# Kernel optimization log

Measured on AMD Instinct MI355X. Metric: run time of the kernel, lower is better.

## Reference

```python
import jax, jax.numpy as jnp
import numpy as np


def _bilinear_sample(fea, px, py):
    # fea: [C,H,W]; px,py: [D,H,W] pixel coords (align_corners=True, zeros padding)
    C, H, W = fea.shape
    x0 = jnp.floor(px); y0 = jnp.floor(py)
    wx = px - x0; wy = py - y0
    x0i = x0.astype(jnp.int32); y0i = y0.astype(jnp.int32)

    def g(xi, yi):
        valid = (xi >= 0) & (xi < W) & (yi >= 0) & (yi < H)
        v = fea[:, jnp.clip(yi, 0, H - 1), jnp.clip(xi, 0, W - 1)]  # [C,D,H,W]
        return jnp.where(valid[None], v, 0.0)

    return (g(x0i, y0i) * ((1 - wx) * (1 - wy))[None]
            + g(x0i + 1, y0i) * (wx * (1 - wy))[None]
            + g(x0i, y0i + 1) * ((1 - wx) * wy)[None]
            + g(x0i + 1, y0i + 1) * (wx * wy)[None])


def homo_warping_3d(src_fea, src_proj, ref_proj, depth_values):
    # src_fea [B,C,H,W]; src_proj/ref_proj [B,4,4]; depth_values [B,D] -> [B,C,D,H,W]
    B, C, H, W = src_fea.shape
    D = depth_values.shape[1]
    proj = src_proj @ jnp.linalg.inv(ref_proj)
    rot, trans = proj[:, :3, :3], proj[:, :3, 3]
    yy, xx = jnp.meshgrid(jnp.arange(H, dtype=src_fea.dtype),
                          jnp.arange(W, dtype=src_fea.dtype), indexing='ij')
    xyz = jnp.stack([xx.ravel(), yy.ravel(), jnp.ones(H * W, src_fea.dtype)], 0)  # [3,HW]
    rot_xyz = jnp.einsum('bij,jp->bip', rot, xyz)  # [B,3,HW]
    pxyz = rot_xyz[:, :, None, :] * depth_values[:, None, :, None] + trans[:, :, None, None]
    xy = pxyz[:, :2] / pxyz[:, 2:3]
    # grid is computed under torch.no_grad() in the original
    px = jax.lax.stop_gradient(xy[:, 0].reshape(B, D, H, W))
    py = jax.lax.stop_gradient(xy[:, 1].reshape(B, D, H, W))
    return jax.vmap(_bilinear_sample)(src_fea, px, py)  # [B,C,D,H,W]


def conf_regression(p, n=4):
    # sliding sum of n consecutive depth probabilities, gathered at expected depth index
    B, D, H, W = p.shape
    pad = jnp.pad(p, ((0, 0), (1, 2), (0, 0), (0, 0)))  # [B,D+3,H,W]
    cs = jnp.cumsum(pad, axis=1)
    cs = jnp.concatenate([jnp.zeros_like(cs[:, :1]), cs], axis=1)  # [B,D+4,H,W]
    sum_n = cs[:, n:n + D] - cs[:, 0:D]  # [B,D,H,W]
    d_idx = jnp.sum(p * jnp.arange(D, dtype=p.dtype)[None, :, None, None], axis=1)
    idx = jnp.clip(d_idx.astype(jnp.int32), 0, D - 1)
    return jnp.take_along_axis(sum_n, idx[:, None], axis=1)[:, 0]


def reference(ref_feats, src_feats, proj_matrices, depth_values, num_depth, w_reg):
    V = proj_matrices.shape[1]
    assert ref_feats.shape[0] == V - 1 and depth_values.shape[1] == num_depth
    ref_proj = proj_matrices[:, 0]
    ref_proj_new = ref_proj[:, 0].at[:, :3, :4].set(ref_proj[:, 1, :3, :3] @ ref_proj[:, 0, :3, :4])
    volume_sum = 0.0
    for v in range(V - 1):
        src_proj = proj_matrices[:, v + 1]
        src_proj_new = src_proj[:, 0].at[:, :3, :4].set(src_proj[:, 1, :3, :3] @ src_proj[:, 0, :3, :4])
        warped = homo_warping_3d(src_feats[v], src_proj_new, ref_proj_new, depth_values)
        volume_sum = volume_sum + ref_feats[v][:, :, None] * warped  # [B,C,D,H,W]
    volume_mean = volume_sum / (V - 1)
    # cost regularization: bias-free 3x3x3 3D conv C->1
    cost = jax.lax.conv_general_dilated(volume_mean, w_reg, (1, 1, 1), 'SAME',
                                        dimension_numbers=('NCDHW', 'OIDHW', 'NCDHW'))
    prob_volume = jax.nn.softmax(cost[:, 0], axis=1)  # [B,D,H,W]
    depth = jnp.sum(prob_volume * depth_values[:, :, None, None], axis=1)  # [B,H,W]
    conf = jax.lax.stop_gradient(conf_regression(prob_volume))  # [B,H,W]
    return depth, conf


def setup_inputs() -> dict:
    key = jax.random.key(0)
    B, V, C, D, H, W = 1, 5, 32, 48, 128, 160
    k1, k2, k3 = jax.random.split(key, 3)
    ref_feats = jax.random.normal(k1, (V - 1, B, C, H, W), jnp.float32)
    src_feats = jax.random.normal(k2, (V - 1, B, C, H, W), jnp.float32)
    # geometrically valid cameras: index 0 = extrinsic 4x4, index 1 = intrinsic 4x4
    f = 200.0
    K = np.eye(4, dtype=np.float32)
    K[0, 0] = f; K[1, 1] = f; K[0, 2] = W / 2.0; K[1, 2] = H / 2.0
    projs = np.zeros((B, V, 2, 4, 4), np.float32)
    for v in range(V):
        ang = 0.04 * v
        R = np.array([[np.cos(ang), 0, np.sin(ang)], [0, 1, 0], [-np.sin(ang), 0, np.cos(ang)]], np.float32)
        E = np.eye(4, dtype=np.float32)
        E[:3, :3] = R
        E[:3, 3] = np.array([-40.0 * v, 0.0, 0.0], np.float32)
        projs[:, v, 0] = E
        projs[:, v, 1] = K
    depth_values = jnp.broadcast_to(jnp.linspace(425.0, 935.0, D, dtype=jnp.float32)[None], (B, D))
    w_reg = jax.random.normal(k3, (1, C, 3, 3, 3), jnp.float32) * 0.05
    return {"ref_feats": ref_feats, "src_feats": src_feats,
            "proj_matrices": jnp.asarray(projs), "depth_values": depth_values,
            "num_depth": D, "w_reg": w_reg}
```

## Files before the change

kernel.cpp:

```cpp
#include <hip/hip_runtime.h>
#include <math.h>

#define H_ 128
#define W_ 160
#define D_ 48
#define C_ 32
#define K27 27
#define HW_ (H_ * W_)
#define DHW_ (D_ * HW_)
#define CHW_ (C_ * HW_)

typedef float f4 __attribute__((ext_vector_type(4)));

__device__ __forceinline__ void build_proj(const float* __restrict__ P, int v,
                                           double M[4][4]) {
    const float* E = P + (v * 2 + 0) * 16;
    const float* K = P + (v * 2 + 1) * 16;
    for (int i = 0; i < 3; i++)
        for (int j = 0; j < 4; j++) {
            double s = 0.0;
            for (int k = 0; k < 3; k++) s += (double)K[i * 4 + k] * (double)E[k * 4 + j];
            M[i][j] = s;
        }
    for (int j = 0; j < 4; j++) M[3][j] = (double)E[12 + j];
}

__global__ void proj_kernel(const float* __restrict__ P, float* __restrict__ rt) {
    if (threadIdx.x != 0) return;
    double M0[4][4];
    build_proj(P, 0, M0);
    double a[4][8];
    for (int i = 0; i < 4; i++)
        for (int j = 0; j < 4; j++) {
            a[i][j] = M0[i][j];
            a[i][4 + j] = (i == j) ? 1.0 : 0.0;
        }
    for (int col = 0; col < 4; ++col) {
        int piv = col;
        double best = fabs(a[col][col]);
        for (int r = col + 1; r < 4; r++) {
            double vv = fabs(a[r][col]);
            if (vv > best) { best = vv; piv = r; }
        }
        if (piv != col)
            for (int j = 0; j < 8; j++) {
                double t = a[col][j]; a[col][j] = a[piv][j]; a[piv][j] = t;
            }
        double inv = 1.0 / a[col][col];
        for (int j = 0; j < 8; j++) a[col][j] *= inv;
        for (int r = 0; r < 4; r++)
            if (r != col) {
                double f = a[r][col];
                for (int j = 0; j < 8; j++) a[r][j] -= f * a[col][j];
            }
    }
    double Minv[4][4];
    for (int i = 0; i < 4; i++)
        for (int j = 0; j < 4; j++) Minv[i][j] = a[i][4 + j];

    for (int v = 1; v < 5; ++v) {
        double Mv[4][4];
        build_proj(P, v, Mv);
        double Pm[4][4];
        for (int i = 0; i < 4; i++)
            for (int j = 0; j < 4; j++) {
                double s = 0.0;
                for (int k = 0; k < 4; k++) s += Mv[i][k] * Minv[k][j];
                Pm[i][j] = s;
            }
        float* o = rt + (v - 1) * 12;
        o[0] = (float)Pm[0][0]; o[1] = (float)Pm[0][1]; o[2] = (float)Pm[0][2];
        o[3] = (float)Pm[1][0]; o[4] = (float)Pm[1][1]; o[5] = (float)Pm[1][2];
        o[6] = (float)Pm[2][0]; o[7] = (float)Pm[2][1]; o[8] = (float)Pm[2][2];
        o[9] = (float)Pm[0][3]; o[10] = (float)Pm[1][3]; o[11] = (float)Pm[2][3];
    }
}

__global__ void transpose_kernel(const float* __restrict__ in,
                                 float* __restrict__ out) {
    int t = blockIdx.x * blockDim.x + threadIdx.x;
    if (t >= 4 * HW_) return;
    int pix = t % HW_;
    int v = t / HW_;
    float vals[C_];
#pragma unroll
    for (int c = 0; c < C_; c++) vals[c] = in[(size_t)v * CHW_ + c * HW_ + pix];
    f4* o = (f4*)(out + ((size_t)v * HW_ + pix) * C_);
#pragma unroll
    for (int q = 0; q < 8; q++) {
        f4 w = {vals[4 * q], vals[4 * q + 1], vals[4 * q + 2], vals[4 * q + 3]};
        o[q] = w;
    }
}

__global__ void __launch_bounds__(256)
warp_fold_x_kernel(const float* __restrict__ srcT,
                   const float* __restrict__ refT,
                   const float* __restrict__ rt,
                   const float* __restrict__ dvals,
                   const float* __restrict__ wreg,
                   float* __restrict__ Gx) {
    __shared__ float accT[8][64][4];
    __shared__ float gLDS[K27][164];

    int t = threadIdx.x;
    int blk = blockIdx.x;
    int d = blk >> 7;
    int y = blk & 127;
    float depth = dvals[d];
    float yf = (float)y;
    int rowbase = d * HW_ + y * W_;

#pragma unroll 1
    for (int b = 0; b < 3; b++) {
        int vox = t >> 2;
        int cgrp = t & 3;
        int vg = b * 64 + vox;
        int x = vg - 1;

        f4 acc0 = (f4){0.f, 0.f, 0.f, 0.f};
        f4 acc1 = (f4){0.f, 0.f, 0.f, 0.f};

        if (x >= 0 && x < W_) {
            float xf = (float)x;
            int pix = y * W_ + x;
#pragma unroll 2
            for (int v = 0; v < 4; v++) {
                const float* m = rt + v * 12;
                float px = fmaf(fmaf(m[0], xf, fmaf(m[1], yf, m[2])), depth, m[9]);
                float py = fmaf(fmaf(m[3], xf, fmaf(m[4], yf, m[5])), depth, m[10]);
                float pz = fmaf(fmaf(m[6], xf, fmaf(m[7], yf, m[8])), depth, m[11]);
                float iz = 1.f / pz;
                px *= iz;
                py *= iz;
                float x0f = floorf(px), y0f = floorf(py);
                float wx = px - x0f, wy = py - y0f;
                int x0 = (int)x0f, y0 = (int)y0f;
                int x1 = x0 + 1, y1 = y0 + 1;

                float w00 = (1.f - wx) * (1.f - wy);
                float w10 = wx * (1.f - wy);
                float w01 = (1.f - wx) * wy;
                float w11 = wx * wy;
                bool vx0 = (x0 >= 0) && (x0 < W_);
                bool vx1 = (x1 >= 0) && (x1 < W_);
                bool vy0 = (y0 >= 0) && (y0 < H_);
                bool vy1 = (y1 >= 0) && (y1 < H_);
                if (!(vx0 && vy0)) w00 = 0.f;
                if (!(vx1 && vy0)) w10 = 0.f;
                if (!(vx0 && vy1)) w01 = 0.f;
                if (!(vx1 && vy1)) w11 = 0.f;
                int cx0 = min(max(x0, 0), W_ - 1);
                int cx1 = min(max(x1, 0), W_ - 1);
                int cy0 = min(max(y0, 0), H_ - 1);
                int cy1 = min(max(y1, 0), H_ - 1);

                const f4* p00 = (const f4*)(srcT + ((size_t)v * HW_ + cy0 * W_ + cx0) * C_ + cgrp * 8);
                const f4* p10 = (const f4*)(srcT + ((size_t)v * HW_ + cy0 * W_ + cx1) * C_ + cgrp * 8);
                const f4* p01 = (const f4*)(srcT + ((size_t)v * HW_ + cy1 * W_ + cx0) * C_ + cgrp * 8);
                const f4* p11 = (const f4*)(srcT + ((size_t)v * HW_ + cy1 * W_ + cx1) * C_ + cgrp * 8);
                const f4* pr  = (const f4*)(refT + ((size_t)v * HW_ + pix) * C_ + cgrp * 8);

                f4 a00 = p00[0], b00 = p00[1];
                f4 a10 = p10[0], b10 = p10[1];
                f4 a01 = p01[0], b01 = p01[1];
                f4 a11 = p11[0], b11 = p11[1];
                f4 r0 = pr[0],  r1 = pr[1];

                f4 sv0 = a00 * w00 + a10 * w10 + a01 * w01 + a11 * w11;
                f4 sv1 = b00 * w00 + b10 * w10 + b01 * w01 + b11 * w11;
                acc0 += r0 * sv0;
                acc1 += r1 * sv1;
            }
            acc0 *= 0.25f;
            acc1 *= 0.25f;
        }

        int cq0 = cgrp * 2;
        *(f4*)&accT[cq0][vox][0] = acc0;
        *(f4*)&accT[cq0 + 1][vox][0] = acc1;
        __syncthreads();

        int fvox = t & 63;
        int kg = t >> 6;
        int fvg = b * 64 + fvox;
        float av[C_];
#pragma unroll
        for (int cq = 0; cq < 8; cq++)
            *(f4*)&av[cq * 4] = *(const f4*)&accT[cq][fvox][0];

        if (fvg < 162) {
            int kstart = kg * 7;
            int kend = min(kstart + 7, K27);
#pragma unroll 1
            for (int k = kstart; k < kend; k++) {
                int ku = __builtin_amdgcn_readfirstlane(k);
                float g = 0.f;
#pragma unroll
                for (int c = 0; c < C_; c++) g = fmaf(wreg[c * K27 + ku], av[c], g);
                gLDS[ku][fvg] = g;
            }
        }
        __syncthreads();
    }

    if (t < W_) {
        int x = t;
#pragma unroll
        for (int j = 0; j < 9; j++) {
            float s = gLDS[j * 3 + 0][x] + gLDS[j * 3 + 1][x + 1] +
                      gLDS[j * 3 + 2][x + 2];
            Gx[(size_t)j * DHW_ + rowbase + x] = s;
        }
    }
}

__global__ void gather9_kernel(const float* __restrict__ Gx,
                               float* __restrict__ cost) {
    int t = blockIdx.x * blockDim.x + threadIdx.x;
    if (t >= DHW_ / 4) return;
    int idx = t * 4;
    int x = idx % W_;
    int y = (idx / W_) % H_;
    int d = idx / HW_;
    f4 acc = (f4){0.f, 0.f, 0.f, 0.f};
#pragma unroll
    for (int kd = 0; kd < 3; kd++) {
        int dd = d + kd - 1;
        if ((unsigned)dd >= (unsigned)D_) continue;
#pragma unroll
        for (int kh = 0; kh < 3; kh++) {
            int yy = y + kh - 1;
            if ((unsigned)yy >= (unsigned)H_) continue;
            int j = kd * 3 + kh;
            acc += *(const f4*)(Gx + (size_t)j * DHW_ + dd * HW_ + yy * W_ + x);
        }
    }
    *(f4*)(cost + idx) = acc;
}

__global__ void softmax_kernel(const float* __restrict__ cost,
                               const float* __restrict__ dvals,
                               float* __restrict__ out) {
    int pix = blockIdx.x * blockDim.x + threadIdx.x;
    if (pix >= HW_) return;
    float mx = -1e30f;
#pragma unroll 1
    for (int d = 0; d < D_; d++) mx = fmaxf(mx, cost[d * HW_ + pix]);
    float s = 0.f, dnum = 0.f, inum = 0.f;
#pragma unroll 1
    for (int d = 0; d < D_; d++) {
        float e = __expf(cost[d * HW_ + pix] - mx);
        s += e;
        dnum = fmaf(e, dvals[d], dnum);
        inum = fmaf(e, (float)d, inum);
    }
    float invs = 1.f / s;
    float depth = dnum * invs;
    float didx = inum * invs;
    int id = (int)didx;
    id = min(max(id, 0), D_ - 1);
    float conf = 0.f;
    for (int k = id - 1; k <= id + 2; ++k)
        if (k >= 0 && k < D_) conf += __expf(cost[k * HW_ + pix] - mx);
    conf *= invs;
    out[pix] = depth;
    out[HW_ + pix] = conf;
}

extern "C" void kernel_launch(void* const* d_in, const int* in_sizes, int n_in,
                              void* d_out, int out_size, void* d_ws, size_t ws_size,
                              hipStream_t stream) {
    const float* ref_feats = (const float*)d_in[0];
    const float* src_feats = (const float*)d_in[1];
    const float* proj      = (const float*)d_in[2];
    const float* dvals     = (const float*)d_in[3];
    const float* wreg      = (const float*)d_in[5];
    float* out = (float*)d_out;

    char* ws = (char*)d_ws;
    float* rt   = (float*)ws;
    float* srcT = (float*)(ws + 1024);
    float* refT = srcT + (size_t)4 * HW_ * C_;
    float* Gx   = refT + (size_t)4 * HW_ * C_;
    float* cost = Gx + (size_t)9 * DHW_;

    proj_kernel<<<1, 64, 0, stream>>>(proj, rt);
    transpose_kernel<<<(4 * HW_) / 256, 256, 0, stream>>>(src_feats, srcT);
    transpose_kernel<<<(4 * HW_) / 256, 256, 0, stream>>>(ref_feats, refT);
    warp_fold_x_kernel<<<D_ * H_, 256, 0, stream>>>(srcT, refT, rt, dvals, wreg, Gx);
    gather9_kernel<<<(DHW_ / 4) / 256, 256, 0, stream>>>(Gx, cost);
    softmax_kernel<<<HW_ / 256, 256, 0, stream>>>(cost, dvals, out);
}
```

Measured before the change: 217.2 us.

## Share per-view warp coordinates via shuffles, merge transposes, vectorize softmax

In the warp kernel, each of the four lanes serving a voxel now computes the projection and bilinear weights and offsets for one view, using per-row constants hoisted out of the loop. The results are broadcast to the other lanes with wave shuffles, so the projection math is not repeated four times per voxel. The two feature transposes become one launch, and the softmax kernel handles four pixels per thread with vector loads. The cost is eight shuffles per view iteration and fewer threads in the softmax, which lowers its parallelism.

Result: faster. 212.4 us (-2.2%).

```diff
diff --git a/kernel.cpp b/kernel.cpp
--- a/kernel.cpp
+++ b/kernel.cpp
@@ -76,10 +76,18 @@
     }
 }
 
-__global__ void transpose_kernel(const float* __restrict__ in,
-                                 float* __restrict__ out) {
+__global__ void transpose2_kernel(const float* __restrict__ sf,
+                                  const float* __restrict__ rf,
+                                  float* __restrict__ so,
+                                  float* __restrict__ ro) {
     int t = blockIdx.x * blockDim.x + threadIdx.x;
-    if (t >= 4 * HW_) return;
+    const float* in = sf;
+    float* out = so;
+    if (t >= 4 * HW_) {
+        t -= 4 * HW_;
+        in = rf;
+        out = ro;
+    }
     int pix = t % HW_;
     int v = t / HW_;
     float vals[C_];
@@ -104,6 +112,10 @@
     __shared__ float gLDS[K27][164];
 
     int t = threadIdx.x;
+    int lane = t & 63;
+    int qb = lane & 60;
+    int vox = t >> 2;
+    int cgrp = t & 3;
     int blk = blockIdx.x;
     int d = blk >> 7;
     int y = blk & 127;
@@ -111,55 +123,77 @@
     float yf = (float)y;
     int rowbase = d * HW_ + y * W_;
 
+    const float* m = rt + cgrp * 12;
+    float Ax = fmaf(fmaf(m[1], yf, m[2]), depth, m[9]);
+    float Bx = m[0] * depth;
+    float Ay = fmaf(fmaf(m[4], yf, m[5]), depth, m[10]);
+    float By = m[3] * depth;
+    float Az = fmaf(fmaf(m[7], yf, m[8]), depth, m[11]);
+    float Bz = m[6] * depth;
+
 #pragma unroll 1
     for (int b = 0; b < 3; b++) {
-        int vox = t >> 2;
-        int cgrp = t & 3;
         int vg = b * 64 + vox;
         int x = vg - 1;
+        bool xvalid = (x >= 0) && (x < W_);
+
+        float W00, W10, W01, W11;
+        int O00, O10, O01, O11;
+        {
+            float xf = (float)x;
+            float pz = fmaf(Bz, xf, Az);
+            float iz = 1.f / pz;
+            float px = fmaf(Bx, xf, Ax) * iz;
+            float py = fmaf(By, xf, Ay) * iz;
+            float x0f = floorf(px), y0f = floorf(py);
+            float wx = px - x0f, wy = py - y0f;
+            int x0 = (int)x0f, y0 = (int)y0f;
+            int x1 = x0 + 1, y1 = y0 + 1;
+            W00 = (1.f - wx) * (1.f - wy);
+            W10 = wx * (1.f - wy);
+            W01 = (1.f - wx) * wy;
+            W11 = wx * wy;
+            bool vx0 = (x0 >= 0) && (x0 < W_);
+            bool vx1 = (x1 >= 0) && (x1 < W_);
+            bool vy0 = (y0 >= 0) && (y0 < H_);
+            bool vy1 = (y1 >= 0) && (y1 < H_);
+            if (!(vx0 && vy0)) W00 = 0.f;
+            if (!(vx1 && vy0)) W10 = 0.f;
+            if (!(vx0 && vy1)) W01 = 0.f;
+            if (!(vx1 && vy1)) W11 = 0.f;
+            int cx0 = min(max(x0, 0), W_ - 1);
+            int cx1 = min(max(x1, 0), W_ - 1);
+            int cy0 = min(max(y0, 0), H_ - 1);
+            int cy1 = min(max(y1, 0), H_ - 1);
+            O00 = (cy0 * W_ + cx0) * C_;
+            O10 = (cy0 * W_ + cx1) * C_;
+            O01 = (cy1 * W_ + cx0) * C_;
+            O11 = (cy1 * W_ + cx1) * C_;
+        }
 
         f4 acc0 = (f4){0.f, 0.f, 0.f, 0.f};
         f4 acc1 = (f4){0.f, 0.f, 0.f, 0.f};
 
-        if (x >= 0 && x < W_) {
-            float xf = (float)x;
+        if (xvalid) {
             int pix = y * W_ + x;
+            const float* rbase = refT + (size_t)pix * C_ + cgrp * 8;
 #pragma unroll 2
             for (int v = 0; v < 4; v++) {
-                const float* m = rt + v * 12;
-                float px = fmaf(fmaf(m[0], xf, fmaf(m[1], yf, m[2])), depth, m[9]);
-                float py = fmaf(fmaf(m[3], xf, fmaf(m[4], yf, m[5])), depth, m[10]);
-                float pz = fmaf(fmaf(m[6], xf, fmaf(m[7], yf, m[8])), depth, m[11]);
-                float iz = 1.f / pz;
-                px *= iz;
-                py *= iz;
-                float x0f = floorf(px), y0f = floorf(py);
-                float wx = px - x0f, wy = py - y0f;
-                int x0 = (int)x0f, y0 = (int)y0f;
-                int x1 = x0 + 1, y1 = y0 + 1;
-
-                float w00 = (1.f - wx) * (1.f - wy);
-                float w10 = wx * (1.f - wy);
-                float w01 = (1.f - wx) * wy;
-                float w11 = wx * wy;
-                bool vx0 = (x0 >= 0) && (x0 < W_);
-                bool vx1 = (x1 >= 0) && (x1 < W_);
-                bool vy0 = (y0 >= 0) && (y0 < H_);
-                bool vy1 = (y1 >= 0) && (y1 < H_);
-                if (!(vx0 && vy0)) w00 = 0.f;
-                if (!(vx1 && vy0)) w10 = 0.f;
-                if (!(vx0 && vy1)) w01 = 0.f;
-                if (!(vx1 && vy1)) w11 = 0.f;
-                int cx0 = min(max(x0, 0), W_ - 1);
-                int cx1 = min(max(x1, 0), W_ - 1);
-                int cy0 = min(max(y0, 0), H_ - 1);
-                int cy1 = min(max(y1, 0), H_ - 1);
-
-                const f4* p00 = (const f4*)(srcT + ((size_t)v * HW_ + cy0 * W_ + cx0) * C_ + cgrp * 8);
-                const f4* p10 = (const f4*)(srcT + ((size_t)v * HW_ + cy0 * W_ + cx1) * C_ + cgrp * 8);
-                const f4* p01 = (const f4*)(srcT + ((size_t)v * HW_ + cy1 * W_ + cx0) * C_ + cgrp * 8);
-                const f4* p11 = (const f4*)(srcT + ((size_t)v * HW_ + cy1 * W_ + cx1) * C_ + cgrp * 8);
-                const f4* pr  = (const f4*)(refT + ((size_t)v * HW_ + pix) * C_ + cgrp * 8);
+                float w00 = __shfl(W00, qb + v);
+                float w10 = __shfl(W10, qb + v);
+                float w01 = __shfl(W01, qb + v);
+                float w11 = __shfl(W11, qb + v);
+                int o00 = __shfl(O00, qb + v);
+                int o10 = __shfl(O10, qb + v);
+                int o01 = __shfl(O01, qb + v);
+                int o11 = __shfl(O11, qb + v);
+
+                const float* sv = srcT + (size_t)v * HW_ * C_ + cgrp * 8;
+                const f4* p00 = (const f4*)(sv + o00);
+                const f4* p10 = (const f4*)(sv + o10);
+                const f4* p01 = (const f4*)(sv + o01);
+                const f4* p11 = (const f4*)(sv + o11);
+                const f4* pr  = (const f4*)(rbase + (size_t)v * HW_ * C_);
 
                 f4 a00 = p00[0], b00 = p00[1];
                 f4 a10 = p10[0], b10 = p10[1];
@@ -242,30 +276,45 @@
 __global__ void softmax_kernel(const float* __restrict__ cost,
                                const float* __restrict__ dvals,
                                float* __restrict__ out) {
-    int pix = blockIdx.x * blockDim.x + threadIdx.x;
-    if (pix >= HW_) return;
-    float mx = -1e30f;
+    int q = blockIdx.x * blockDim.x + threadIdx.x;
+    if (q >= HW_ / 4) return;
+    int base = q * 4;
+
+    f4 mx = (f4){-1e30f, -1e30f, -1e30f, -1e30f};
+#pragma unroll 8
+    for (int d = 0; d < D_; d++) {
+        f4 c = *(const f4*)(cost + (size_t)d * HW_ + base);
+#pragma unroll
+        for (int j = 0; j < 4; j++) mx[j] = fmaxf(mx[j], c[j]);
+    }
+    f4 s = (f4){0.f, 0.f, 0.f, 0.f};
+    f4 dn = (f4){0.f, 0.f, 0.f, 0.f};
+    f4 in = (f4){0.f, 0.f, 0.f, 0.f};
+#pragma unroll 8
+    for (int d = 0; d < D_; d++) {
+        f4 c = *(const f4*)(cost + (size_t)d * HW_ + base);
+        float dv = dvals[d];
+#pragma unroll
+        for (int j = 0; j < 4; j++) {
+            float e = __expf(c[j] - mx[j]);
+            s[j] += e;
+            dn[j] = fmaf(e, dv, dn[j]);
+            in[j] = fmaf(e, (float)d, in[j]);
+        }
+    }
+#pragma unroll
+    for (int j = 0; j < 4; j++) {
+        float invs = 1.f / s[j];
+        float depth = dn[j] * invs;
+        int id = (int)(in[j] * invs);
+        id = min(max(id, 0), D_ - 1);
+        float conf = 0.f;
 #pragma unroll 1
-    for (int d = 0; d < D_; d++) mx = fmaxf(mx, cost[d * HW_ + pix]);
-    float s = 0.f, dnum = 0.f, inum = 0.f;
-#pragma unroll 1
-    for (int d = 0; d < D_; d++) {
-        float e = __expf(cost[d * HW_ + pix] - mx);
-        s += e;
-        dnum = fmaf(e, dvals[d], dnum);
-        inum = fmaf(e, (float)d, inum);
-    }
-    float invs = 1.f / s;
-    float depth = dnum * invs;
-    float didx = inum * invs;
-    int id = (int)didx;
-    id = min(max(id, 0), D_ - 1);
-    float conf = 0.f;
-    for (int k = id - 1; k <= id + 2; ++k)
-        if (k >= 0 && k < D_) conf += __expf(cost[k * HW_ + pix] - mx);
-    conf *= invs;
-    out[pix] = depth;
-    out[HW_ + pix] = conf;
+        for (int k = id - 1; k <= id + 2; ++k)
+            if (k >= 0 && k < D_) conf += __expf(cost[(size_t)k * HW_ + base + j] - mx[j]);
+        out[base + j] = depth;
+        out[HW_ + base + j] = conf * invs;
+    }
 }
 
 extern "C" void kernel_launch(void* const* d_in, const int* in_sizes, int n_in,
@@ -286,9 +335,9 @@
     float* cost = Gx + (size_t)9 * DHW_;
 
     proj_kernel<<<1, 64, 0, stream>>>(proj, rt);
-    transpose_kernel<<<(4 * HW_) / 256, 256, 0, stream>>>(src_feats, srcT);
-    transpose_kernel<<<(4 * HW_) / 256, 256, 0, stream>>>(ref_feats, refT);
+    transpose2_kernel<<<(8 * HW_) / 256, 256, 0, stream>>>(src_feats, ref_feats,
+                                                           srcT, refT);
     warp_fold_x_kernel<<<D_ * H_, 256, 0, stream>>>(srcT, refT, rt, dvals, wreg, Gx);
     gather9_kernel<<<(DHW_ / 4) / 256, 256, 0, stream>>>(Gx, cost);
-    softmax_kernel<<<HW_ / 256, 256, 0, stream>>>(cost, dvals, out);
-}
+    softmax_kernel<<<(HW_ / 4) / 256, 256, 0, stream>>>(cost, dvals, out);
+}
```
